# Performance work log

Hardware: AMD Instinct MI355X
Metric: run time of the kernel (lower is better)

## Reference

```python
import jax, jax.numpy as jnp
import numpy as np
import math

B, L, D = 2, 2048, 1024
H = 16
DH = D // H  # 64
XPOS_SCALE_BASE = 512.0
THETA = 10000.0


def setup_inputs() -> dict:
    key = jax.random.key(0)
    ks = jax.random.split(key, 9)
    s = 0.02  # keep logits in a sane range like trained weights
    return {
        "x": jax.random.normal(ks[0], (B, L, D), dtype=jnp.float32),
        "Wq": jax.random.normal(ks[1], (D, D), dtype=jnp.float32) * s,
        "bq": jax.random.normal(ks[2], (D,), dtype=jnp.float32) * s,
        "Wk": jax.random.normal(ks[3], (D, D), dtype=jnp.float32) * s,
        "bk": jax.random.normal(ks[4], (D,), dtype=jnp.float32) * s,
        "Wv": jax.random.normal(ks[5], (D, D), dtype=jnp.float32) * s,
        "bv": jax.random.normal(ks[6], (D,), dtype=jnp.float32) * s,
        "Wo": jax.random.normal(ks[7], (D, D), dtype=jnp.float32) * s,
        "bo": jax.random.normal(ks[8], (D,), dtype=jnp.float32) * s,
    }


def _rotate_half(t):
    # pairwise interleaved rotation, as in rotary_embedding_torch
    t1 = t[..., 0::2]
    t2 = t[..., 1::2]
    return jnp.stack([-t2, t1], axis=-1).reshape(t.shape)


def _xpos_rotate(q, k):
    # q, k: [B, H, L, DH]; xPos rotary embedding (use_xpos=True)
    seq = q.shape[2]
    half = jnp.arange(0, DH, 2, dtype=jnp.float32)
    inv_freq = 1.0 / (THETA ** (half / DH))            # [DH/2]
    t = jnp.arange(seq, dtype=jnp.float32)             # [L]
    freqs = t[:, None] * inv_freq[None, :]             # [L, DH/2]
    freqs = jnp.repeat(freqs, 2, axis=-1)              # [L, DH] interleaved
    # xPos length-extrapolatable scale
    scale_vec = (half + 0.4 * DH) / (1.4 * DH)         # [DH/2]
    power = (t - seq // 2) / XPOS_SCALE_BASE           # [L]
    scale = scale_vec[None, :] ** power[:, None]       # [L, DH/2]
    scale = jnp.repeat(scale, 2, axis=-1)              # [L, DH]
    cos = jnp.cos(freqs)
    sin = jnp.sin(freqs)
    q_out = q * (cos * scale) + _rotate_half(q) * (sin * scale)
    k_out = k * (cos / scale) + _rotate_half(k) * (sin / scale)
    return q_out, k_out


def reference(x, Wq, bq, Wk, bk, Wv, bv, Wo, bo):
    b, l, d = x.shape
    # projections; note source swaps names: v_mat <- k-proj, k_mat <- v-proj
    q = (x @ Wq.T + bq).reshape(b, l, H, DH).transpose(0, 2, 1, 3)  # [b,h,l,dh]
    v = (x @ Wk.T + bk).reshape(b, l, H, DH).transpose(0, 2, 1, 3)
    k = (x @ Wv.T + bv).reshape(b, l, H, DH).transpose(0, 2, 1, 3)
    q, k = _xpos_rotate(q, k)
    # source divides by sqrt(Dh * num_heads) == sqrt(dim)
    scores = jnp.einsum("bhqd,bhkd->bhqk", q, k) / math.sqrt(d)
    weights = jax.nn.softmax(scores, axis=-1)
    inter = jnp.einsum("bhqk,bhkd->bhqd", weights, v)
    inter = inter.transpose(0, 2, 1, 3).reshape(b, l, d)
    return inter @ Wo.T + bo
```

## Files before the change

### kernel.cpp

```cpp
#include <hip/hip_runtime.h>
#include <math.h>

#define NB 2
#define NL 2048
#define ND 1024
#define NH 16
#define NDH 64
#define NBL 4096

typedef __attribute__((ext_vector_type(4)))  float f32x4;
typedef __attribute__((ext_vector_type(16))) float f32x16;
typedef __attribute__((ext_vector_type(8)))  short s16x8;
typedef __attribute__((ext_vector_type(4)))  short s16x4;

#define LOG2E 1.44269504088896f

__device__ __forceinline__ float fexp2(float x){
#if __has_builtin(__builtin_amdgcn_exp2f)
  return __builtin_amdgcn_exp2f(x);
#else
  return exp2f(x);
#endif
}

__device__ __forceinline__ unsigned short f2bf(float f){
  unsigned int u = __float_as_uint(f);
  u += 0x7FFF + ((u >> 16) & 1);
  return (unsigned short)(u >> 16);
}

__device__ __forceinline__ unsigned int pk2bf(float lo, float hi){
  return __builtin_amdgcn_perm(__float_as_uint(hi) + 0x8000u,
                               __float_as_uint(lo) + 0x8000u, 0x07060302u);
}

__global__ void cvt_all(const float* __restrict__ x,
                        const float* __restrict__ wq, const float* __restrict__ wk,
                        const float* __restrict__ wv, const float* __restrict__ wo,
                        unsigned short* __restrict__ xb,
                        unsigned short* __restrict__ wqb, unsigned short* __restrict__ wkb,
                        unsigned short* __restrict__ wvb, unsigned short* __restrict__ wob){
  int i = blockIdx.x * blockDim.x + threadIdx.x;
  const float* s; unsigned short* d; int off;
  if (i < (1<<20)) { s = x; d = xb; off = i; }
  else {
    int j = i - (1<<20); int w = j >> 18; off = j & ((1<<18)-1);
    s = (w==0)?wq:(w==1)?wk:(w==2)?wv:wo;
    d = (w==0)?wqb:(w==1)?wkb:(w==2)?wvb:wob;
  }
  float4 f = reinterpret_cast<const float4*>(s)[off];
  ushort4 r; r.x=f2bf(f.x); r.y=f2bf(f.y); r.z=f2bf(f.z); r.w=f2bf(f.w);
  reinterpret_cast<ushort4*>(d)[off] = r;
}

__global__ void rope_tables(float2* __restrict__ qtab, float2* __restrict__ ktab){
  int t = blockIdx.x * blockDim.x + threadIdx.x;
  int l = t >> 5, i = t & 31;
  float half = 2.0f * (float)i;
  float inv_freq = 1.0f / powf(10000.0f, half / 64.0f);
  float fr = (float)l * inv_freq;
  float sv = (half + 0.4f * 64.0f) / (1.4f * 64.0f);
  float pw = ((float)l - 1024.0f) / 512.0f;
  float sc = powf(sv, pw);
  float cs = cosf(fr), sn = sinf(fr);
  qtab[t] = make_float2(cs * sc, sn * sc);
  ktab[t] = make_float2(cs / sc, sn / sc);
}

__device__ __forceinline__ void gemm_core128(
    const unsigned short* __restrict__ A, const unsigned short* __restrict__ W,
    int row0, int col0,
    unsigned short (&As)[128][32], unsigned short (&Bs)[128][32],
    f32x4 (&acc)[4][4])
{
  const int tid  = threadIdx.x;
  const int wave = tid >> 6, lane = tid & 63;
  const int m16  = lane & 15, quad = lane >> 4;
  const int mrow = (wave & 1) * 64, ncol = (wave >> 1) * 64;
  const int rA   = lane >> 2, cA = (lane & 3) * 8;

  for (int k0 = 0; k0 < ND; k0 += 32){
    __syncthreads();
#pragma unroll
    for (int i2 = 0; i2 < 2; i2++){
      const int c = wave * 2 + i2;
      const unsigned short* ga = A + (size_t)(row0 + c*16 + rA) * ND + k0 + cA;
      const unsigned short* gb = W + (size_t)(col0 + c*16 + rA) * ND + k0 + cA;
      __builtin_amdgcn_global_load_lds((const __attribute__((address_space(1))) void*)ga,
                                       (__attribute__((address_space(3))) void*)&As[c*16][0], 16, 0, 0);
      __builtin_amdgcn_global_load_lds((const __attribute__((address_space(1))) void*)gb,
                                       (__attribute__((address_space(3))) void*)&Bs[c*16][0], 16, 0, 0);
    }
    __syncthreads();
    s16x8 af[4], bf[4];
#pragma unroll
    for (int mt = 0; mt < 4; mt++) af[mt] = *reinterpret_cast<const s16x8*>(&As[mrow + mt*16 + m16][quad*8]);
#pragma unroll
    for (int nt = 0; nt < 4; nt++) bf[nt] = *reinterpret_cast<const s16x8*>(&Bs[ncol + nt*16 + m16][quad*8]);
#pragma unroll
    for (int mt = 0; mt < 4; mt++)
#pragma unroll
      for (int nt = 0; nt < 4; nt++)
        acc[mt][nt] = __builtin_amdgcn_mfma_f32_16x16x32_bf16(af[mt], bf[nt], acc[mt][nt], 0, 0, 0);
  }
}

__global__ __launch_bounds__(256) void gemm_qkv(
    const unsigned short* __restrict__ A,
    const unsigned short* __restrict__ Wq, const float* __restrict__ bq,
    const unsigned short* __restrict__ Wk, const float* __restrict__ bk,
    const unsigned short* __restrict__ Wv, const float* __restrict__ bv,
    unsigned short* __restrict__ qb, unsigned short* __restrict__ kb,
    unsigned short* __restrict__ vtb,
    const float2* __restrict__ qtab, const float2* __restrict__ ktab)
{
  __shared__ unsigned short As[128][32];
  __shared__ unsigned short Bs[128][32];
  __shared__ unsigned short T[128][72];

  const int mode = blockIdx.z;
  const unsigned short* W = (mode==0) ? Wq : (mode==1) ? Wk : Wv;
  const float* bias       = (mode==0) ? bq : (mode==1) ? bk : bv;

  const int row0 = blockIdx.x * 128, col0 = blockIdx.y * 128;
  f32x4 acc[4][4] = {};
  gemm_core128(A, W, row0, col0, As, Bs, acc);

  const int tid  = threadIdx.x;
  const int wave = tid >> 6, lane = tid & 63;
  const int m16  = lane & 15, quad = lane >> 4;
  const int mrow = (wave & 1) * 64, ncol = (wave >> 1) * 64;

  if (mode == 2){
    const int b = row0 >> 11, l0 = row0 & (NL - 1);
#pragma unroll
    for (int h2 = 0; h2 < 2; h2++){
      __syncthreads();
      if ((wave >> 1) == h2){
#pragma unroll
        for (int mt = 0; mt < 4; mt++)
#pragma unroll
          for (int nt = 0; nt < 4; nt++)
#pragma unroll
            for (int r = 0; r < 4; r++){
              int lrow = mrow + mt*16 + quad*4 + r;
              int dh   = nt*16 + m16;
              T[lrow][dh] = f2bf(acc[mt][nt][r] + bias[col0 + h2*64 + dh]);
            }
      }
      __syncthreads();
      const int bh = b * NH + (col0 >> 6) + h2;
#pragma unroll
      for (int j4 = 0; j4 < 4; j4++){
        int c = tid * 4 + j4;
        int d = c >> 4, seg = (c & 15) * 8;
        unsigned short tmp[8];
#pragma unroll
        for (int jj = 0; jj < 8; jj++) tmp[jj] = T[seg + jj][d];
        *reinterpret_cast<uint4*>(vtb + (size_t)(bh * NDH + d) * NL + l0 + seg) =
            *reinterpret_cast<uint4*>(tmp);
      }
    }
  } else {
    const float qscale = (mode == 0) ? (0.03125f * LOG2E) : 1.0f;
    const float2* tab  = (mode == 0) ? qtab : ktab;
    unsigned short* dst = (mode == 0) ? qb : kb;
#pragma unroll
    for (int mt = 0; mt < 4; mt++)
#pragma unroll
      for (int nt = 0; nt < 4; nt++)
#pragma unroll
        for (int r = 0; r < 4; r++){
          int grow = row0 + mrow + mt*16 + quad*4 + r;
          int gcol = col0 + ncol + nt*16 + m16;
          float v = acc[mt][nt][r] + bias[gcol];
          int b = grow >> 11, l = grow & (NL - 1);
          int h = gcol >> 6, dh = gcol & 63;
          float pv = __shfl_xor(v, 1);
          float2 t = tab[l*32 + (dh >> 1)];
          float rh = (dh & 1) ? pv : -pv;
          float ov = (v * t.x + rh * t.y) * qscale;
          dst[(((size_t)(b * NH + h)) * NL + l) * NDH + dh] = f2bf(ov);
        }
  }
}

__global__ __launch_bounds__(256) void gemm_o(
    const unsigned short* __restrict__ A, const unsigned short* __restrict__ W,
    const float* __restrict__ bias, float* __restrict__ out)
{
  __shared__ unsigned short As[128][32];
  __shared__ unsigned short Bs[64][32];
  const int tid  = threadIdx.x;
  const int wave = tid >> 6, lane = tid & 63;
  const int m16  = lane & 15, quad = lane >> 4;
  const int mrow = (wave & 1) * 64, ncol = (wave >> 1) * 32;
  const int rA   = lane >> 2, cA = (lane & 3) * 8;
  const int row0 = blockIdx.x * 128, col0 = blockIdx.y * 64;

  f32x4 acc[4][2] = {};

  for (int k0 = 0; k0 < ND; k0 += 32){
    __syncthreads();
#pragma unroll
    for (int i3 = 0; i3 < 3; i3++){
      const int c = wave * 3 + i3;
      const unsigned short* g; unsigned short* l;
      if (c < 8){ g = A + (size_t)(row0 + c*16 + rA) * ND + k0 + cA;      l = &As[c*16][0]; }
      else      { g = W + (size_t)(col0 + (c-8)*16 + rA) * ND + k0 + cA;  l = &Bs[(c-8)*16][0]; }
      __builtin_amdgcn_global_load_lds((const __attribute__((address_space(1))) void*)g,
                                       (__attribute__((address_space(3))) void*)l, 16, 0, 0);
    }
    __syncthreads();
    s16x8 af[4], bf[2];
#pragma unroll
    for (int mt = 0; mt < 4; mt++) af[mt] = *reinterpret_cast<const s16x8*>(&As[mrow + mt*16 + m16][quad*8]);
#pragma unroll
    for (int nt = 0; nt < 2; nt++) bf[nt] = *reinterpret_cast<const s16x8*>(&Bs[ncol + nt*16 + m16][quad*8]);
#pragma unroll
    for (int mt = 0; mt < 4; mt++)
#pragma unroll
      for (int nt = 0; nt < 2; nt++)
        acc[mt][nt] = __builtin_amdgcn_mfma_f32_16x16x32_bf16(af[mt], bf[nt], acc[mt][nt], 0, 0, 0);
  }

#pragma unroll
  for (int mt = 0; mt < 4; mt++)
#pragma unroll
    for (int nt = 0; nt < 2; nt++)
#pragma unroll
      for (int r = 0; r < 4; r++){
        int grow = row0 + mrow + mt*16 + quad*4 + r;
        int gcol = col0 + ncol + nt*16 + m16;
        out[(size_t)grow * ND + gcol] = acc[mt][nt][r] + bias[gcol];
      }
}

__global__ __launch_bounds__(256, 2) void attn_kernel(
    const unsigned short* __restrict__ qb,
    const unsigned short* __restrict__ kb,
    const unsigned short* __restrict__ vtb,
    unsigned short* __restrict__ opart,
    float* __restrict__ lsum)
{
  __shared__ unsigned short smem[256 * 72];
  const int tid  = threadIdx.x;
  const int wave = tid >> 6, lane = tid & 63;
  const int l31  = lane & 31, g = lane >> 5;
  const int bh   = blockIdx.y;
  const int z    = blockIdx.z;
  const int q0   = blockIdx.x * 256;
  const int kbase = z * (NL / 2);
  const unsigned short* Q  = qb  + (size_t)bh * NL * NDH;
  const unsigned short* K  = kb  + (size_t)bh * NL * NDH;
  const unsigned short* Vt = vtb + (size_t)bh * NDH * NL;

  s16x8 qf[2][4];
#pragma unroll
  for (int q2 = 0; q2 < 2; q2++)
#pragma unroll
    for (int s = 0; s < 4; s++)
      qf[q2][s] = *reinterpret_cast<const s16x8*>(
          Q + (size_t)(q0 + wave*64 + q2*32 + l31) * NDH + s*16 + g*8);

  const int r0 = tid >> 3, c0 = tid & 7;
  const int r1 = r0 + 32;
  const int so0 = r0*64 + ((c0 ^ (r0 & 7)) * 8);
  const int so1 = r1*64 + ((c0 ^ (r1 & 7)) * 8);

  uint4 kreg0 = *reinterpret_cast<const uint4*>(K  + (size_t)(kbase + r0) * NDH + c0*8);
  uint4 kreg1 = *reinterpret_cast<const uint4*>(K  + (size_t)(kbase + r1) * NDH + c0*8);
  uint4 vreg0 = *reinterpret_cast<const uint4*>(Vt + (size_t)r0 * NL + kbase + c0*8);
  uint4 vreg1 = *reinterpret_cast<const uint4*>(Vt + (size_t)r1 * NL + kbase + c0*8);
  *reinterpret_cast<uint4*>(&smem[so0])         = kreg0;
  *reinterpret_cast<uint4*>(&smem[so1])         = kreg1;
  *reinterpret_cast<uint4*>(&smem[8192 + so0])  = vreg0;
  *reinterpret_cast<uint4*>(&smem[8192 + so1])  = vreg1;
  kreg0 = *reinterpret_cast<const uint4*>(K  + (size_t)(kbase + 64 + r0) * NDH + c0*8);
  kreg1 = *reinterpret_cast<const uint4*>(K  + (size_t)(kbase + 64 + r1) * NDH + c0*8);
  vreg0 = *reinterpret_cast<const uint4*>(Vt + (size_t)r0 * NL + kbase + 64 + c0*8);
  vreg1 = *reinterpret_cast<const uint4*>(Vt + (size_t)r1 * NL + kbase + 64 + c0*8);
  __syncthreads();

  float ls[2] = {0.f, 0.f};
  f32x16 ot[2][2] = {};
  const int key7 = l31 & 7;

  for (int kt = 0; kt < 16; kt++){
    const int cur = (kt & 1) * 4096;
    const int nxt = 4096 - cur;
    if (kt < 15){
      *reinterpret_cast<uint4*>(&smem[nxt + so0])        = kreg0;
      *reinterpret_cast<uint4*>(&smem[nxt + so1])        = kreg1;
      *reinterpret_cast<uint4*>(&smem[8192 + nxt + so0]) = vreg0;
      *reinterpret_cast<uint4*>(&smem[8192 + nxt + so1]) = vreg1;
    }
    if (kt < 14){
      const int k0n = kbase + (kt + 2) * 64;
      kreg0 = *reinterpret_cast<const uint4*>(K  + (size_t)(k0n + r0) * NDH + c0*8);
      kreg1 = *reinterpret_cast<const uint4*>(K  + (size_t)(k0n + r1) * NDH + c0*8);
      vreg0 = *reinterpret_cast<const uint4*>(Vt + (size_t)r0 * NL + k0n + c0*8);
      vreg1 = *reinterpret_cast<const uint4*>(Vt + (size_t)r1 * NL + k0n + c0*8);
    }

    const unsigned short* Kb = &smem[cur];
    const unsigned short* Vb = &smem[8192 + cur];

    uint2 pmat[2][8];
#pragma unroll
    for (int t = 0; t < 2; t++){
      f32x16 st0 = {}, st1 = {};
#pragma unroll
      for (int s = 0; s < 4; s++){
        const int cg = (2*s + g) ^ key7;
        s16x8 kf = *reinterpret_cast<const s16x8*>(&Kb[(t*32 + l31)*64 + cg*8]);
        st0 = __builtin_amdgcn_mfma_f32_32x32x16_bf16(kf, qf[0][s], st0, 0, 0, 0);
        st1 = __builtin_amdgcn_mfma_f32_32x32x16_bf16(kf, qf[1][s], st1, 0, 0, 0);
      }
#pragma unroll
      for (int j = 0; j < 4; j++){
        float a0 = fexp2(st0[4*j]), a1 = fexp2(st0[4*j+1]);
        float a2 = fexp2(st0[4*j+2]), a3 = fexp2(st0[4*j+3]);
        ls[0] += (a0 + a1) + (a2 + a3);
        pmat[0][t*4+j].x = pk2bf(a0, a1);
        pmat[0][t*4+j].y = pk2bf(a2, a3);
        float b0 = fexp2(st1[4*j]), b1 = fexp2(st1[4*j+1]);
        float b2 = fexp2(st1[4*j+2]), b3 = fexp2(st1[4*j+3]);
        ls[1] += (b0 + b1) + (b2 + b3);
        pmat[1][t*4+j].x = pk2bf(b0, b1);
        pmat[1][t*4+j].y = pk2bf(b2, b3);
      }
    }

#pragma unroll
    for (int mt = 0; mt < 2; mt++){
      const int dh = mt*32 + l31;
#pragma unroll
      for (int s = 0; s < 8; s++){
        const int cg = s ^ (dh & 7);
        s16x4 vf = *reinterpret_cast<const s16x4*>(&Vb[dh*64 + cg*8 + g*4]);
        ot[mt][0] = __builtin_amdgcn_mfma_f32_32x32x8bf16_1k(
            vf, *reinterpret_cast<s16x4*>(&pmat[0][s]), ot[mt][0], 0, 0, 0);
        ot[mt][1] = __builtin_amdgcn_mfma_f32_32x32x8bf16_1k(
            vf, *reinterpret_cast<s16x4*>(&pmat[1][s]), ot[mt][1], 0, 0, 0);
      }
    }
    __syncthreads();
  }

#pragma unroll
  for (int q2 = 0; q2 < 2; q2++){
    float t = ls[q2] + __shfl_xor(ls[q2], 32);
    if (g == 0)
      lsum[((size_t)z * NB * NH + bh) * NL + q0 + wave*64 + q2*32 + l31] = t;
  }

#pragma unroll
  for (int mt = 0; mt < 2; mt++)
#pragma unroll
    for (int q2 = 0; q2 < 2; q2++)
#pragma unroll
      for (int s = 0; s < 4; s++){
        uint2 pk;
        pk.x = pk2bf(ot[mt][q2][4*s], ot[mt][q2][4*s + 1]);
        pk.y = pk2bf(ot[mt][q2][4*s + 2], ot[mt][q2][4*s + 3]);
        *reinterpret_cast<uint2*>(&smem[(wave*64 + q2*32 + l31)*72 + mt*32 + s*8 + g*4]) = pk;
      }
  __syncthreads();

  const int bb = bh >> 4, h = bh & 15;
  unsigned short* od = opart + (size_t)z * NBL * ND;
#pragma unroll
  for (int j = 0; j < 8; j++){
    int idx = j*256 + tid;
    int row = idx >> 3, cg2 = (idx & 7) * 8;
    *reinterpret_cast<uint4*>(od + ((size_t)(bb*NL + q0 + row)) * ND + h*NDH + cg2) =
        *reinterpret_cast<const uint4*>(&smem[row*72 + cg2]);
  }
}

__device__ __forceinline__ unsigned int comb2(unsigned int a, unsigned int b, float inv){
  float alo = __uint_as_float(a << 16), ahi = __uint_as_float(a & 0xFFFF0000u);
  float blo = __uint_as_float(b << 16), bhi = __uint_as_float(b & 0xFFFF0000u);
  return pk2bf((alo + blo) * inv, (ahi + bhi) * inv);
}

__global__ __launch_bounds__(256) void attn_combine(
    unsigned short* __restrict__ opart, const float* __restrict__ lsum)
{
  int idx = blockIdx.x * 256 + threadIdx.x;
  int row = idx >> 7;
  int col8 = idx & 127;
  int h = col8 >> 3;
  int b = row >> 11, l = row & (NL - 1);
  int bh = b * NH + h;
  float l0 = lsum[(size_t)bh * NL + l];
  float l1 = lsum[(size_t)(NB*NH + bh) * NL + l];
  float inv = 1.0f / (l0 + l1);
  uint4 u0 = reinterpret_cast<const uint4*>(opart)[idx];
  uint4 u1 = reinterpret_cast<const uint4*>(opart + (size_t)NBL * ND)[idx];
  uint4 o;
  o.x = comb2(u0.x, u1.x, inv);
  o.y = comb2(u0.y, u1.y, inv);
  o.z = comb2(u0.z, u1.z, inv);
  o.w = comb2(u0.w, u1.w, inv);
  reinterpret_cast<uint4*>(opart)[idx] = o;
}

extern "C" void kernel_launch(void* const* d_in, const int* in_sizes, int n_in,
                              void* d_out, int out_size, void* d_ws, size_t ws_size,
                              hipStream_t stream)
{
  (void)in_sizes; (void)n_in; (void)out_size; (void)ws_size;
  const float* x  = (const float*)d_in[0];
  const float* Wq = (const float*)d_in[1];
  const float* bq = (const float*)d_in[2];
  const float* Wk = (const float*)d_in[3];
  const float* bk = (const float*)d_in[4];
  const float* Wv = (const float*)d_in[5];
  const float* bv = (const float*)d_in[6];
  const float* Wo = (const float*)d_in[7];
  const float* bo = (const float*)d_in[8];
  float* out = (float*)d_out;

  char* p = (char*)d_ws;
  unsigned short* xb    = (unsigned short*)p; p += (size_t)NBL*ND*2;
  unsigned short* wqb   = (unsigned short*)p; p += (size_t)ND*ND*2;
  unsigned short* wkb   = (unsigned short*)p; p += (size_t)ND*ND*2;
  unsigned short* wvb   = (unsigned short*)p; p += (size_t)ND*ND*2;
  unsigned short* wob   = (unsigned short*)p; p += (size_t)ND*ND*2;
  unsigned short* qbuf  = (unsigned short*)p; p += (size_t)NBL*ND*2;
  unsigned short* kbuf  = (unsigned short*)p; p += (size_t)NBL*ND*2;
  unsigned short* vtb   = (unsigned short*)p; p += (size_t)NBL*ND*2;
  unsigned short* opart = (unsigned short*)p; p += (size_t)2*NBL*ND*2;
  float* lsum = (float*)p; p += (size_t)2*NB*NH*NL*4;
  float2* qtab = (float2*)p; p += (size_t)NL*32*8;
  float2* ktab = (float2*)p; p += (size_t)NL*32*8;

  hipLaunchKernelGGL(cvt_all, dim3(8192), dim3(256), 0, stream,
                     x, Wq, Wk, Wv, Wo, xb, wqb, wkb, wvb, wob);
  hipLaunchKernelGGL(rope_tables, dim3(NL*32/256), dim3(256), 0, stream, qtab, ktab);

  hipLaunchKernelGGL(gemm_qkv, dim3(NBL/128, ND/128, 3), dim3(256), 0, stream,
                     xb, wqb, bq, wvb, bv, wkb, bk, qbuf, kbuf, vtb, qtab, ktab);

  hipLaunchKernelGGL(attn_kernel, dim3(NL/256, NB*NH, 2), dim3(256), 0, stream,
                     qbuf, kbuf, vtb, opart, lsum);
  hipLaunchKernelGGL(attn_combine, dim3(NBL*ND/8/256), dim3(256), 0, stream, opart, lsum);

  hipLaunchKernelGGL(gemm_o, dim3(NBL/128, ND/64), dim3(256), 0, stream, opart, wob, bo, out);
}
```

Measured before the change: 207.7 us.

## Shrink QKV GEMM tile to one head, stage epilogue in LDS, fuse rope tables

The QKV projection GEMM now uses 128x64 tiles, one head per block, with a single shared LDS buffer reused for operand staging and the epilogue. Q and K results are written to LDS and then stored as coalesced 16-byte rows, replacing scattered 2-byte global stores. Launch bounds request 4 blocks per CU. The rope table generation is folded into the conversion kernel, which removes one launch. The tradeoff is doubled grid size and lower per-block operand reuse, in exchange for higher occupancy and better store coalescing.

```diff
diff --git a/kernel.cpp b/kernel.cpp
--- a/kernel.cpp
+++ b/kernel.cpp
@@ -39,73 +39,36 @@
                         const float* __restrict__ wv, const float* __restrict__ wo,
                         unsigned short* __restrict__ xb,
                         unsigned short* __restrict__ wqb, unsigned short* __restrict__ wkb,
-                        unsigned short* __restrict__ wvb, unsigned short* __restrict__ wob){
+                        unsigned short* __restrict__ wvb, unsigned short* __restrict__ wob,
+                        float2* __restrict__ qtab, float2* __restrict__ ktab){
   int i = blockIdx.x * blockDim.x + threadIdx.x;
-  const float* s; unsigned short* d; int off;
-  if (i < (1<<20)) { s = x; d = xb; off = i; }
-  else {
-    int j = i - (1<<20); int w = j >> 18; off = j & ((1<<18)-1);
-    s = (w==0)?wq:(w==1)?wk:(w==2)?wv:wo;
-    d = (w==0)?wqb:(w==1)?wkb:(w==2)?wvb:wob;
-  }
-  float4 f = reinterpret_cast<const float4*>(s)[off];
-  ushort4 r; r.x=f2bf(f.x); r.y=f2bf(f.y); r.z=f2bf(f.z); r.w=f2bf(f.w);
-  reinterpret_cast<ushort4*>(d)[off] = r;
-}
-
-__global__ void rope_tables(float2* __restrict__ qtab, float2* __restrict__ ktab){
-  int t = blockIdx.x * blockDim.x + threadIdx.x;
-  int l = t >> 5, i = t & 31;
-  float half = 2.0f * (float)i;
-  float inv_freq = 1.0f / powf(10000.0f, half / 64.0f);
-  float fr = (float)l * inv_freq;
-  float sv = (half + 0.4f * 64.0f) / (1.4f * 64.0f);
-  float pw = ((float)l - 1024.0f) / 512.0f;
-  float sc = powf(sv, pw);
-  float cs = cosf(fr), sn = sinf(fr);
-  qtab[t] = make_float2(cs * sc, sn * sc);
-  ktab[t] = make_float2(cs / sc, sn / sc);
-}
-
-__device__ __forceinline__ void gemm_core128(
-    const unsigned short* __restrict__ A, const unsigned short* __restrict__ W,
-    int row0, int col0,
-    unsigned short (&As)[128][32], unsigned short (&Bs)[128][32],
-    f32x4 (&acc)[4][4])
-{
-  const int tid  = threadIdx.x;
-  const int wave = tid >> 6, lane = tid & 63;
-  const int m16  = lane & 15, quad = lane >> 4;
-  const int mrow = (wave & 1) * 64, ncol = (wave >> 1) * 64;
-  const int rA   = lane >> 2, cA = (lane & 3) * 8;
-
-  for (int k0 = 0; k0 < ND; k0 += 32){
-    __syncthreads();
-#pragma unroll
-    for (int i2 = 0; i2 < 2; i2++){
-      const int c = wave * 2 + i2;
-      const unsigned short* ga = A + (size_t)(row0 + c*16 + rA) * ND + k0 + cA;
-      const unsigned short* gb = W + (size_t)(col0 + c*16 + rA) * ND + k0 + cA;
-      __builtin_amdgcn_global_load_lds((const __attribute__((address_space(1))) void*)ga,
-                                       (__attribute__((address_space(3))) void*)&As[c*16][0], 16, 0, 0);
-      __builtin_amdgcn_global_load_lds((const __attribute__((address_space(1))) void*)gb,
-                                       (__attribute__((address_space(3))) void*)&Bs[c*16][0], 16, 0, 0);
-    }
-    __syncthreads();
-    s16x8 af[4], bf[4];
-#pragma unroll
-    for (int mt = 0; mt < 4; mt++) af[mt] = *reinterpret_cast<const s16x8*>(&As[mrow + mt*16 + m16][quad*8]);
-#pragma unroll
-    for (int nt = 0; nt < 4; nt++) bf[nt] = *reinterpret_cast<const s16x8*>(&Bs[ncol + nt*16 + m16][quad*8]);
-#pragma unroll
-    for (int mt = 0; mt < 4; mt++)
-#pragma unroll
-      for (int nt = 0; nt < 4; nt++)
-        acc[mt][nt] = __builtin_amdgcn_mfma_f32_16x16x32_bf16(af[mt], bf[nt], acc[mt][nt], 0, 0, 0);
-  }
-}
-
-__global__ __launch_bounds__(256) void gemm_qkv(
+  if (i < (1<<21)){
+    const float* s; unsigned short* d; int off;
+    if (i < (1<<20)) { s = x; d = xb; off = i; }
+    else {
+      int j = i - (1<<20); int w = j >> 18; off = j & ((1<<18)-1);
+      s = (w==0)?wq:(w==1)?wk:(w==2)?wv:wo;
+      d = (w==0)?wqb:(w==1)?wkb:(w==2)?wvb:wob;
+    }
+    float4 f = reinterpret_cast<const float4*>(s)[off];
+    ushort4 r; r.x=f2bf(f.x); r.y=f2bf(f.y); r.z=f2bf(f.z); r.w=f2bf(f.w);
+    reinterpret_cast<ushort4*>(d)[off] = r;
+  } else {
+    int t = i - (1<<21);
+    int l = t >> 5, k = t & 31;
+    float half = 2.0f * (float)k;
+    float inv_freq = 1.0f / powf(10000.0f, half / 64.0f);
+    float fr = (float)l * inv_freq;
+    float sv = (half + 0.4f * 64.0f) / (1.4f * 64.0f);
+    float pw = ((float)l - 1024.0f) / 512.0f;
+    float sc = powf(sv, pw);
+    float cs = cosf(fr), sn = sinf(fr);
+    qtab[t] = make_float2(cs * sc, sn * sc);
+    ktab[t] = make_float2(cs / sc, sn / sc);
+  }
+}
+
+__global__ __launch_bounds__(256, 4) void gemm_qkv(
     const unsigned short* __restrict__ A,
     const unsigned short* __restrict__ Wq, const float* __restrict__ bq,
     const unsigned short* __restrict__ Wk, const float* __restrict__ bk,
@@ -114,74 +77,103 @@
     unsigned short* __restrict__ vtb,
     const float2* __restrict__ qtab, const float2* __restrict__ ktab)
 {
-  __shared__ unsigned short As[128][32];
-  __shared__ unsigned short Bs[128][32];
-  __shared__ unsigned short T[128][72];
+  __shared__ unsigned short smem[9216];
 
   const int mode = blockIdx.z;
   const unsigned short* W = (mode==0) ? Wq : (mode==1) ? Wk : Wv;
   const float* bias       = (mode==0) ? bq : (mode==1) ? bk : bv;
 
-  const int row0 = blockIdx.x * 128, col0 = blockIdx.y * 128;
-  f32x4 acc[4][4] = {};
-  gemm_core128(A, W, row0, col0, As, Bs, acc);
-
   const int tid  = threadIdx.x;
   const int wave = tid >> 6, lane = tid & 63;
   const int m16  = lane & 15, quad = lane >> 4;
-  const int mrow = (wave & 1) * 64, ncol = (wave >> 1) * 64;
+  const int mrow = (wave & 1) * 64, ncol = (wave >> 1) * 32;
+  const int rA   = lane >> 2, cA = (lane & 3) * 8;
+  const int row0 = blockIdx.x * 128, col0 = blockIdx.y * 64;
+
+  f32x4 acc[4][2] = {};
+
+  for (int k0 = 0; k0 < ND; k0 += 32){
+    __syncthreads();
+#pragma unroll
+    for (int i3 = 0; i3 < 3; i3++){
+      const int c = wave * 3 + i3;
+      const unsigned short* g; unsigned short* l;
+      if (c < 8){ g = A + (size_t)(row0 + c*16 + rA) * ND + k0 + cA;      l = &smem[c*512]; }
+      else      { g = W + (size_t)(col0 + (c-8)*16 + rA) * ND + k0 + cA;  l = &smem[4096 + (c-8)*512]; }
+      __builtin_amdgcn_global_load_lds((const __attribute__((address_space(1))) void*)g,
+                                       (__attribute__((address_space(3))) void*)l, 16, 0, 0);
+    }
+    __syncthreads();
+    s16x8 af[4], bf[2];
+#pragma unroll
+    for (int mt = 0; mt < 4; mt++)
+      af[mt] = *reinterpret_cast<const s16x8*>(&smem[(mrow + mt*16 + m16)*32 + quad*8]);
+#pragma unroll
+    for (int nt = 0; nt < 2; nt++)
+      bf[nt] = *reinterpret_cast<const s16x8*>(&smem[4096 + (ncol + nt*16 + m16)*32 + quad*8]);
+#pragma unroll
+    for (int mt = 0; mt < 4; mt++)
+#pragma unroll
+      for (int nt = 0; nt < 2; nt++)
+        acc[mt][nt] = __builtin_amdgcn_mfma_f32_16x16x32_bf16(af[mt], bf[nt], acc[mt][nt], 0, 0, 0);
+  }
+  __syncthreads();
+
+  const int b  = row0 >> 11, l0 = row0 & (NL - 1);
+  const int h  = col0 >> 6;
+  const int bh = b * NH + h;
 
   if (mode == 2){
-    const int b = row0 >> 11, l0 = row0 & (NL - 1);
-#pragma unroll
-    for (int h2 = 0; h2 < 2; h2++){
-      __syncthreads();
-      if ((wave >> 1) == h2){
-#pragma unroll
-        for (int mt = 0; mt < 4; mt++)
-#pragma unroll
-          for (int nt = 0; nt < 4; nt++)
-#pragma unroll
-            for (int r = 0; r < 4; r++){
-              int lrow = mrow + mt*16 + quad*4 + r;
-              int dh   = nt*16 + m16;
-              T[lrow][dh] = f2bf(acc[mt][nt][r] + bias[col0 + h2*64 + dh]);
-            }
-      }
-      __syncthreads();
-      const int bh = b * NH + (col0 >> 6) + h2;
-#pragma unroll
-      for (int j4 = 0; j4 < 4; j4++){
-        int c = tid * 4 + j4;
-        int d = c >> 4, seg = (c & 15) * 8;
-        unsigned short tmp[8];
-#pragma unroll
-        for (int jj = 0; jj < 8; jj++) tmp[jj] = T[seg + jj][d];
-        *reinterpret_cast<uint4*>(vtb + (size_t)(bh * NDH + d) * NL + l0 + seg) =
-            *reinterpret_cast<uint4*>(tmp);
-      }
-    }
+#pragma unroll
+    for (int mt = 0; mt < 4; mt++)
+#pragma unroll
+      for (int nt = 0; nt < 2; nt++)
+#pragma unroll
+        for (int r = 0; r < 4; r++){
+          int lrow = mrow + mt*16 + quad*4 + r;
+          int dhl  = ncol + nt*16 + m16;
+          smem[lrow*72 + dhl] = f2bf(acc[mt][nt][r] + bias[col0 + dhl]);
+        }
   } else {
     const float qscale = (mode == 0) ? (0.03125f * LOG2E) : 1.0f;
     const float2* tab  = (mode == 0) ? qtab : ktab;
-    unsigned short* dst = (mode == 0) ? qb : kb;
 #pragma unroll
     for (int mt = 0; mt < 4; mt++)
 #pragma unroll
-      for (int nt = 0; nt < 4; nt++)
+      for (int nt = 0; nt < 2; nt++)
 #pragma unroll
         for (int r = 0; r < 4; r++){
-          int grow = row0 + mrow + mt*16 + quad*4 + r;
-          int gcol = col0 + ncol + nt*16 + m16;
-          float v = acc[mt][nt][r] + bias[gcol];
-          int b = grow >> 11, l = grow & (NL - 1);
-          int h = gcol >> 6, dh = gcol & 63;
+          int lrow = mrow + mt*16 + quad*4 + r;
+          int dhl  = ncol + nt*16 + m16;
+          float v  = acc[mt][nt][r] + bias[col0 + dhl];
           float pv = __shfl_xor(v, 1);
-          float2 t = tab[l*32 + (dh >> 1)];
-          float rh = (dh & 1) ? pv : -pv;
-          float ov = (v * t.x + rh * t.y) * qscale;
-          dst[(((size_t)(b * NH + h)) * NL + l) * NDH + dh] = f2bf(ov);
+          float2 t = tab[(l0 + lrow)*32 + (dhl >> 1)];
+          float rh = (dhl & 1) ? pv : -pv;
+          smem[lrow*72 + dhl] = f2bf((v * t.x + rh * t.y) * qscale);
         }
+  }
+  __syncthreads();
+
+  if (mode == 2){
+#pragma unroll
+    for (int j4 = 0; j4 < 4; j4++){
+      int c = tid * 4 + j4;
+      int d = c >> 4, seg = (c & 15) * 8;
+      unsigned short tmp[8];
+#pragma unroll
+      for (int jj = 0; jj < 8; jj++) tmp[jj] = smem[(seg + jj)*72 + d];
+      *reinterpret_cast<uint4*>(vtb + (size_t)(bh * NDH + d) * NL + l0 + seg) =
+          *reinterpret_cast<uint4*>(tmp);
+    }
+  } else {
+    unsigned short* dst = ((mode == 0) ? qb : kb) + ((size_t)bh * NL + l0) * NDH;
+#pragma unroll
+    for (int j = 0; j < 4; j++){
+      int idx = j*256 + tid;
+      int row = idx >> 3, cg = (idx & 7) * 8;
+      *reinterpret_cast<uint4*>(dst + row*NDH + cg) =
+          *reinterpret_cast<const uint4*>(&smem[row*72 + cg]);
+    }
   }
 }
 
@@ -437,11 +429,10 @@
   float2* qtab = (float2*)p; p += (size_t)NL*32*8;
   float2* ktab = (float2*)p; p += (size_t)NL*32*8;
 
-  hipLaunchKernelGGL(cvt_all, dim3(8192), dim3(256), 0, stream,
-                     x, Wq, Wk, Wv, Wo, xb, wqb, wkb, wvb, wob);
-  hipLaunchKernelGGL(rope_tables, dim3(NL*32/256), dim3(256), 0, stream, qtab, ktab);
-
-  hipLaunchKernelGGL(gemm_qkv, dim3(NBL/128, ND/128, 3), dim3(256), 0, stream,
+  hipLaunchKernelGGL(cvt_all, dim3(8448), dim3(256), 0, stream,
+                     x, Wq, Wk, Wv, Wo, xb, wqb, wkb, wvb, wob, qtab, ktab);
+
+  hipLaunchKernelGGL(gemm_qkv, dim3(NBL/128, ND/64, 3), dim3(256), 0, stream,
                      xb, wqb, bq, wvb, bv, wkb, bk, qbuf, kbuf, vtb, qtab, ktab);
 
   hipLaunchKernelGGL(attn_kernel, dim3(NL/256, NB*NH, 2), dim3(256), 0, stream,
```

Result: no change. 208.1 us (+0.2%).
